# Kernel tuning notes

Hardware: AMD Instinct MI355X
Metric: run time of the kernel (lower is better)

## Reference

```python
import jax, jax.numpy as jnp
import numpy as np

N_NODES, N_EDGES, F_IN = 8192, 32768, 16
N_SUB, N_GRAPH = 512, 32
EDGE_DIM, HID = 5, 128
DIMS = [(16, 32), (32, 64), (64, 64)]  # (M_in, M_out) per NNConv layer


def _segment_mean(x, seg, n):
    s = jax.ops.segment_sum(x, seg, num_segments=n)
    c = jax.ops.segment_sum(jnp.ones((x.shape[0], 1), x.dtype), seg, num_segments=n)
    return s / jnp.maximum(c, 1.0)


def _nnconv(x, src, dst, eattr, W1, b1, W2, b2, root, bias):
    # edge MLP -> per-edge weight matrix theta: [E, M_in, M_out]
    h = jax.nn.relu(eattr @ W1 + b1)
    theta = (h @ W2 + b2).reshape(-1, x.shape[1], root.shape[1])
    msg = jnp.einsum('ei,eio->eo', x[src], theta)          # gather + per-edge matvec
    agg = jax.ops.segment_sum(msg, dst, num_segments=x.shape[0])  # scatter-add (aggr='add')
    return agg + x @ root + bias


def setup_inputs() -> dict:
    key = jax.random.key(0)
    ks = jax.random.split(key, 32)
    inp = {}
    inp['x'] = jax.random.normal(ks[0], (N_NODES, F_IN), jnp.float32)
    inp['edge_index'] = jax.random.randint(ks[1], (2, N_EDGES), 0, N_NODES)
    inp['edge_attr'] = jax.random.uniform(ks[2], (N_EDGES, EDGE_DIM), jnp.float32)
    inp['node_to_subgraph'] = jnp.sort(jax.random.randint(ks[3], (N_NODES,), 0, N_SUB))
    inp['subgraph_to_graph'] = jnp.sort(jax.random.randint(ks[4], (N_SUB,), 0, N_GRAPH))
    i = 5
    for l, (ci, co) in enumerate(DIMS):
        inp[f'W1_{l}'] = jax.random.normal(ks[i], (EDGE_DIM, HID), jnp.float32) * 0.1
        inp[f'b1_{l}'] = jnp.zeros((HID,), jnp.float32)
        inp[f'W2_{l}'] = jax.random.normal(ks[i + 1], (HID, ci * co), jnp.float32) * 0.05
        inp[f'b2_{l}'] = jnp.zeros((ci * co,), jnp.float32)
        inp[f'root_{l}'] = jax.random.normal(ks[i + 2], (ci, co), jnp.float32) * 0.1
        inp[f'bias_{l}'] = jnp.zeros((co,), jnp.float32)
        i += 3
    inp['fc1_w'] = jax.random.normal(ks[i], (64, 32), jnp.float32) * 0.1
    inp['fc1_b'] = jnp.zeros((32,), jnp.float32)
    inp['fc2_w'] = jax.random.normal(ks[i + 1], (32, 16), jnp.float32) * 0.1
    inp['fc2_b'] = jnp.zeros((16,), jnp.float32)
    inp['fc3_w'] = jax.random.normal(ks[i + 2], (16, 1), jnp.float32) * 0.1
    inp['fc3_b'] = jnp.zeros((1,), jnp.float32)
    return inp


def reference(x, edge_index, edge_attr, node_to_subgraph, subgraph_to_graph,
              W1_0, b1_0, W2_0, b2_0, root_0, bias_0,
              W1_1, b1_1, W2_1, b2_1, root_1, bias_1,
              W1_2, b1_2, W2_2, b2_2, root_2, bias_2,
              fc1_w, fc1_b, fc2_w, fc2_b, fc3_w, fc3_b):
    src, dst = edge_index[0], edge_index[1]
    layers = [(W1_0, b1_0, W2_0, b2_0, root_0, bias_0),
              (W1_1, b1_1, W2_1, b2_1, root_1, bias_1),
              (W1_2, b1_2, W2_2, b2_2, root_2, bias_2)]
    h = x
    for (W1, b1, W2, b2, root, bias) in layers:
        h = jax.nn.elu(_nnconv(h, src, dst, edge_attr, W1, b1, W2, b2, root, bias))
    h = _segment_mean(h, node_to_subgraph, N_SUB)      # global_mean_pool over subgraphs
    h = _segment_mean(h, subgraph_to_graph, N_GRAPH)   # global_mean_pool over graphs
    h = jax.nn.elu(h @ fc1_w + fc1_b)
    h = jax.nn.elu(h @ fc2_w + fc2_b)
    return (h @ fc3_w + fc3_b).reshape(-1)
```

## Files before the change

kernel.cpp:

```cpp
#include <hip/hip_runtime.h>

#define E_EDGES 32768
#define NN 8192
#define HID 128
#define KS 4

typedef _Float16 half8 __attribute__((ext_vector_type(8)));
typedef _Float16 half4 __attribute__((ext_vector_type(4)));
typedef float f32x4 __attribute__((ext_vector_type(4)));

__global__ void csr_scan_k(const int* __restrict__ dst, float* __restrict__ pools,
                           int npool, int* __restrict__ roff, int* __restrict__ cursor) {
  __shared__ int h[NN];
  __shared__ int ps[1024];
  int t = threadIdx.x;
  for (int j = t; j < NN; j += 1024) h[j] = 0;
  for (int j = t; j < npool; j += 1024) pools[j] = 0.f;
  __syncthreads();
  for (int j = t; j < E_EDGES; j += 1024) atomicAdd(&h[dst[j]], 1);
  __syncthreads();
  int loc[8]; int s = 0;
  int base = t * 8;
#pragma unroll
  for (int j = 0; j < 8; ++j) { loc[j] = s; s += h[base + j]; }
  ps[t] = s;
  __syncthreads();
  for (int off = 1; off < 1024; off <<= 1) {
    int v = 0;
    if (t >= off) v = ps[t - off];
    __syncthreads();
    if (t >= off) ps[t] += v;
    __syncthreads();
  }
  int excl = (t == 0) ? 0 : ps[t - 1];
#pragma unroll
  for (int j = 0; j < 8; ++j) { int v = excl + loc[j]; roff[base + j] = v; cursor[base + j] = v; }
  if (t == 1023) roff[NN] = ps[1023];
}

__global__ void scatter_k(const int* __restrict__ dst, int* __restrict__ cursor, int* __restrict__ eidx) {
  int e = blockIdx.x * 256 + threadIdx.x;
  if (e < E_EDGES) { int p = atomicAdd(&cursor[dst[e]], 1); eidx[p] = e; }
}

__device__ __forceinline__ void prep_one(int idx, int l2ci, int l2co,
                                         const float* __restrict__ W2,
                                         const float* __restrict__ b2,
                                         _Float16* __restrict__ out) {
  int CI = 1 << l2ci, CO = 1 << l2co;
  int Kmain = CI << 7;
  int j = idx & 7;
  int n = (idx >> 3) & (CO - 1);
  int kg = idx >> (3 + l2co);
  int k = kg * 8 + j;
  float v = 0.f;
  if (k < Kmain) {
    int hh = k >> l2ci, i = k & (CI - 1);
    v = W2[((hh << l2ci) + i) * CO + n];
  } else if (k < Kmain + CI) {
    v = b2[(k - Kmain) * CO + n];
  }
  out[idx] = (_Float16)v;
}

__global__ void prep_all_k(const float* __restrict__ W2a, const float* __restrict__ b2a, _Float16* __restrict__ oa,
                           const float* __restrict__ W2b, const float* __restrict__ b2b, _Float16* __restrict__ ob,
                           const float* __restrict__ W2c, const float* __restrict__ b2c, _Float16* __restrict__ oc) {
  const int s0 = 2176 * 32, s1 = 4224 * 64, s2 = 8320 * 64;
  int idx = blockIdx.x * 256 + threadIdx.x;
  if (idx < s0) prep_one(idx, 4, 5, W2a, b2a, oa);
  else if (idx < s0 + s1) prep_one(idx - s0, 5, 6, W2b, b2b, ob);
  else if (idx < s0 + s1 + s2) prep_one(idx - s0 - s1, 6, 6, W2c, b2c, oc);
}

template <int CI, int CO>
__launch_bounds__(256, 2)
__global__ void msg_mfma_k(const float* __restrict__ xcur, const int* __restrict__ src,
                           const float* __restrict__ eattr, const float* __restrict__ W1,
                           const float* __restrict__ b1, const _Float16* __restrict__ Bsw,
                           float* __restrict__ msgbuf) {
  constexpr int ME = 256;
  constexpr int L2CI = (CI == 64) ? 6 : ((CI == 32) ? 5 : 4);
  constexpr int Kmain = 128 * CI;
  constexpr int SPLITK = 32 * CI;
  constexpr int TAILK = ((SPLITK + CI + 127) / 128) * 128;
  constexpr int XSTR = CI + 8;
  constexpr int FC = CO / 16;
  constexpr int C4 = CI / 4;
  constexpr int L2C4 = L2CI - 2;
  constexpr int NV = (CI == 64) ? 2 : 1;

  __shared__ _Float16 he_s[32 * ME];
  __shared__ _Float16 xs_s[ME * XSTR];
  __shared__ float ea_s[ME * 5];
  __shared__ float W1s[5 * 32];
  __shared__ float b1s[32];
  __shared__ int src_s[ME];

  int t = threadIdx.x;
  int e0 = blockIdx.x * ME;
  int y = blockIdx.y;
  int hbeg = y * 32;

  for (int j = t; j < ME * 5; j += 256) ea_s[j] = eattr[e0 * 5 + j];
  if (t < 5 * 32) W1s[t] = W1[(t >> 5) * HID + hbeg + (t & 31)];
  if (t < 32) b1s[t] = b1[hbeg + t];
  src_s[t] = src[e0 + t];
  __syncthreads();

  for (int j = t; j < 32 * ME; j += 256) {
    int hl = j / ME, e = j & (ME - 1);
    float v = b1s[hl];
#pragma unroll
    for (int d = 0; d < 5; ++d) v += ea_s[e * 5 + d] * W1s[d * 32 + hl];
    he_s[hl * ME + e] = (_Float16)fmaxf(v, 0.f);
  }
  for (int j = t; j < ME * C4; j += 256) {
    int e = j >> L2C4, i4 = j & (C4 - 1);
    float4 v = ((const float4*)xcur)[src_s[e] * C4 + i4];
    half4 hq = {(_Float16)v.x, (_Float16)v.y, (_Float16)v.z, (_Float16)v.w};
    *(half4*)&xs_s[e * XSTR + i4 * 4] = hq;
  }
  __syncthreads();

  int lane = t & 63;
  int w = t >> 6;
  int quad = lane >> 4, l15 = lane & 15;

  half8 xreg[4][NV];
#pragma unroll
  for (int fr = 0; fr < 4; ++fr)
#pragma unroll
    for (int v = 0; v < NV; ++v)
      xreg[fr][v] = *(const half8*)&xs_s[(w * 64 + fr * 16 + l15) * XSTR +
                                         ((quad * 8 + v * 32) & (CI - 1))];

  int cbeg = y * (SPLITK / 32);
  int cend = cbeg + ((y < 3) ? (SPLITK / 32) : (TAILK / 32));
  int nrounds = (cend - cbeg) >> 2;

  const half8* bsw8 = (const half8*)Bsw;
  int ib = quad * CO + l15;

  f32x4 acc[4][FC];
#pragma unroll
  for (int fr = 0; fr < 4; ++fr)
#pragma unroll
    for (int fc = 0; fc < FC; ++fc)
#pragma unroll
      for (int r = 0; r < 4; ++r) acc[fr][fc][r] = 0.f;

  half8 breg[4][FC];
#pragma unroll
  for (int j = 0; j < 4; ++j)
#pragma unroll
    for (int fc = 0; fc < FC; ++fc)
      breg[j][fc] = bsw8[(cbeg + j) * 4 * CO + ib + fc * 16];

  for (int r = 0; r < nrounds; ++r) {
#pragma unroll
    for (int j = 0; j < 4; ++j) {
      int c = cbeg + r * 4 + j;
      int kq = c * 32 + quad * 8;
      int hr = (kq >> L2CI) - hbeg;
      constexpr int PAR = (CI == 64) ? 1 : 0;
      int vi = PAR ? (j & 1) : 0;
      half8 a[4];
#pragma unroll
      for (int fr = 0; fr < 4; ++fr) {
        int e = w * 64 + fr * 16 + l15;
        _Float16 hv = (_Float16)1.f;
        if (kq < Kmain) hv = he_s[hr * ME + e];
        a[fr] = xreg[fr][vi] * hv;
      }
#pragma unroll
      for (int fc = 0; fc < FC; ++fc) {
#pragma unroll
        for (int fr = 0; fr < 4; ++fr)
          acc[fr][fc] = __builtin_amdgcn_mfma_f32_16x16x32_f16(a[fr], breg[j][fc], acc[fr][fc], 0, 0, 0);
      }
      int cn = c + 4;
      if (cn >= cend) cn = cend - 1;
#pragma unroll
      for (int fc = 0; fc < FC; ++fc)
        breg[j][fc] = bsw8[cn * 4 * CO + ib + fc * 16];
    }
  }

  float* mb = msgbuf + ((size_t)y * E_EDGES + e0) * CO;
#pragma unroll
  for (int fr = 0; fr < 4; ++fr)
#pragma unroll
    for (int fc = 0; fc < FC; ++fc)
#pragma unroll
      for (int r = 0; r < 4; ++r) {
        int el = w * 64 + fr * 16 + quad * 4 + r;
        int o = fc * 16 + l15;
        mb[el * CO + o] = acc[fr][fc][r];
      }
}

template <int CI, int CO>
__global__ void gather_elu_k(const float* __restrict__ xcur, const float* __restrict__ root,
                             const float* __restrict__ bias, const float* __restrict__ msgbuf,
                             const int* __restrict__ roff, const int* __restrict__ eidx,
                             float* __restrict__ xnext) {
  constexpr int NB = 256 / CO;
  __shared__ float xs[NB * CI];
  int t = threadIdx.x;
  int n0 = blockIdx.x * NB;
  for (int j = t; j < NB * CI; j += 256) xs[j] = xcur[n0 * CI + j];
  __syncthreads();
  int nl = t / CO, o = t & (CO - 1);
  int n = n0 + nl;
  float a = bias[o];
#pragma unroll
  for (int i = 0; i < CI; ++i) a += xs[nl * CI + i] * root[i * CO + o];
  int j1 = roff[n + 1];
  for (int j = roff[n]; j < j1; ++j) {
    int e = eidx[j];
    float m = 0.f;
#pragma unroll
    for (int s = 0; s < KS; ++s) m += msgbuf[((size_t)s * E_EDGES + e) * CO + o];
    a += m;
  }
  xnext[n * CO + o] = a > 0.f ? a : expm1f(a);
}

__global__ void pool_sub_k(const float* __restrict__ x3, const int* __restrict__ n2s,
                           float* __restrict__ ssum, float* __restrict__ scnt) {
  int idx = blockIdx.x * 256 + threadIdx.x;
  int n = idx >> 6, o = idx & 63;
  int s = n2s[n];
  atomicAdd(&ssum[(s << 6) + o], x3[idx]);
  if (o == 0) atomicAdd(&scnt[s], 1.f);
}

__global__ void pool_graph_k(const float* __restrict__ ssum, const float* __restrict__ scnt,
                             const int* __restrict__ s2g, float* __restrict__ gsum,
                             float* __restrict__ gcnt) {
  int idx = blockIdx.x * 256 + threadIdx.x;
  int s = idx >> 6, o = idx & 63;
  int g = s2g[s];
  float v = ssum[idx] / fmaxf(scnt[s], 1.f);
  atomicAdd(&gsum[(g << 6) + o], v);
  if (o == 0) atomicAdd(&gcnt[g], 1.f);
}

__global__ void head_k(const float* __restrict__ gsum, const float* __restrict__ gcnt,
                       const float* __restrict__ w1, const float* __restrict__ b1,
                       const float* __restrict__ w2, const float* __restrict__ b2,
                       const float* __restrict__ w3, const float* __restrict__ b3,
                       float* __restrict__ out) {
  int g = blockIdx.x;
  int t = threadIdx.x;
  __shared__ float m[64], s1[32], s2[16];
  float c = fmaxf(gcnt[g], 1.f);
  m[t] = gsum[g * 64 + t] / c;
  __syncthreads();
  if (t < 32) {
    float a = b1[t];
    for (int i = 0; i < 64; ++i) a += m[i] * w1[i * 32 + t];
    s1[t] = a > 0.f ? a : expm1f(a);
  }
  __syncthreads();
  if (t < 16) {
    float a = b2[t];
    for (int i = 0; i < 32; ++i) a += s1[i] * w2[i * 16 + t];
    s2[t] = a > 0.f ? a : expm1f(a);
  }
  __syncthreads();
  if (t == 0) {
    float a = b3[0];
    for (int i = 0; i < 16; ++i) a += s2[i] * w3[i];
    out[g] = a;
  }
}

extern "C" void kernel_launch(void* const* d_in, const int* in_sizes, int n_in,
                              void* d_out, int out_size, void* d_ws, size_t ws_size,
                              hipStream_t stream) {
  (void)in_sizes; (void)n_in; (void)out_size; (void)ws_size;
  const float* x0 = (const float*)d_in[0];
  const int* ei = (const int*)d_in[1];
  const float* ea = (const float*)d_in[2];
  const int* n2s = (const int*)d_in[3];
  const int* s2g = (const int*)d_in[4];
  const float* W1_[3] = {(const float*)d_in[5], (const float*)d_in[11], (const float*)d_in[17]};
  const float* b1_[3] = {(const float*)d_in[6], (const float*)d_in[12], (const float*)d_in[18]};
  const float* W2_[3] = {(const float*)d_in[7], (const float*)d_in[13], (const float*)d_in[19]};
  const float* b2_[3] = {(const float*)d_in[8], (const float*)d_in[14], (const float*)d_in[20]};
  const float* rt_[3] = {(const float*)d_in[9], (const float*)d_in[15], (const float*)d_in[21]};
  const float* bs_[3] = {(const float*)d_in[10], (const float*)d_in[16], (const float*)d_in[22]};
  const float* fc1w = (const float*)d_in[23]; const float* fc1b = (const float*)d_in[24];
  const float* fc2w = (const float*)d_in[25]; const float* fc2b = (const float*)d_in[26];
  const float* fc3w = (const float*)d_in[27]; const float* fc3b = (const float*)d_in[28];
  float* out = (float*)d_out;

  const int* srcp = ei;
  const int* dstp = ei + E_EDGES;

  char* wsb = (char*)d_ws;
  size_t off = 0;
  auto alloc = [&](size_t bytes) {
    void* p = wsb + off;
    off += (bytes + 255) & ~(size_t)255;
    return p;
  };
  _Float16* Bsw0 = (_Float16*)alloc((size_t)2176 * 32 * 2);
  _Float16* Bsw1 = (_Float16*)alloc((size_t)4224 * 64 * 2);
  _Float16* Bsw2 = (_Float16*)alloc((size_t)8320 * 64 * 2);
  float* msgbuf = (float*)alloc((size_t)KS * E_EDGES * 64 * 4);
  float* x1 = (float*)alloc((size_t)NN * 32 * 4);
  float* x2 = (float*)alloc((size_t)NN * 64 * 4);
  float* x3 = (float*)alloc((size_t)NN * 64 * 4);
  int* roff = (int*)alloc((size_t)(NN + 1) * 4);
  int* cursor = (int*)alloc((size_t)NN * 4);
  int* eidx = (int*)alloc((size_t)E_EDGES * 4);
  const int npool = 512 * 64 + 512 + 32 * 64 + 32;
  float* pools = (float*)alloc((size_t)npool * 4);
  float* ssum = pools;
  float* scnt = pools + 512 * 64;
  float* gsum = scnt + 512;
  float* gcnt = gsum + 32 * 64;

  csr_scan_k<<<1, 1024, 0, stream>>>(dstp, pools, npool, roff, cursor);
  scatter_k<<<E_EDGES / 256, 256, 0, stream>>>(dstp, cursor, eidx);
  const int preptot = 2176 * 32 + 4224 * 64 + 8320 * 64;
  prep_all_k<<<(preptot + 255) / 256, 256, 0, stream>>>(W2_[0], b2_[0], Bsw0,
                                                        W2_[1], b2_[1], Bsw1,
                                                        W2_[2], b2_[2], Bsw2);

  dim3 mg(E_EDGES / 256, KS);
  msg_mfma_k<16, 32><<<mg, 256, 0, stream>>>(x0, srcp, ea, W1_[0], b1_[0], Bsw0, msgbuf);
  gather_elu_k<16, 32><<<NN / 8, 256, 0, stream>>>(x0, rt_[0], bs_[0], msgbuf, roff, eidx, x1);
  msg_mfma_k<32, 64><<<mg, 256, 0, stream>>>(x1, srcp, ea, W1_[1], b1_[1], Bsw1, msgbuf);
  gather_elu_k<32, 64><<<NN / 4, 256, 0, stream>>>(x1, rt_[1], bs_[1], msgbuf, roff, eidx, x2);
  msg_mfma_k<64, 64><<<mg, 256, 0, stream>>>(x2, srcp, ea, W1_[2], b1_[2], Bsw2, msgbuf);
  gather_elu_k<64, 64><<<NN / 4, 256, 0, stream>>>(x2, rt_[2], bs_[2], msgbuf, roff, eidx, x3);

  pool_sub_k<<<NN * 64 / 256, 256, 0, stream>>>(x3, n2s, ssum, scnt);
  pool_graph_k<<<512 * 64 / 256, 256, 0, stream>>>(ssum, scnt, s2g, gsum, gcnt);
  head_k<<<32, 64, 0, stream>>>(gsum, gcnt, fc1w, fc1b, fc2w, fc2b, fc3w, fc3b, out);
}
```

Before: 271.1 us.

## Replace CSR gather with atomic scatter-add from MFMA message kernel, fuse pooling and head

Drops the CSR build (histogram scan plus scatter) and the split-K message buffer. The MFMA message kernel now atomically adds its per-edge results straight into per-layer node aggregation buffers indexed by dst. The finalize kernel reads the aggregate, adds the root term and applies ELU. On the last layer it atomically pools into subgraph sums, and one final kernel computes counts by binary search and runs the graph pooling and MLP head. The aim is to cut kernel launches and msgbuf write/read traffic, at the cost of many global float atomics (4 split-K partial writes per output element) and non-deterministic summation order.

```diff
diff --git a/kernel.cpp b/kernel.cpp
--- a/kernel.cpp
+++ b/kernel.cpp
@@ -3,45 +3,10 @@
 #define E_EDGES 32768
 #define NN 8192
 #define HID 128
-#define KS 4
 
 typedef _Float16 half8 __attribute__((ext_vector_type(8)));
 typedef _Float16 half4 __attribute__((ext_vector_type(4)));
 typedef float f32x4 __attribute__((ext_vector_type(4)));
-
-__global__ void csr_scan_k(const int* __restrict__ dst, float* __restrict__ pools,
-                           int npool, int* __restrict__ roff, int* __restrict__ cursor) {
-  __shared__ int h[NN];
-  __shared__ int ps[1024];
-  int t = threadIdx.x;
-  for (int j = t; j < NN; j += 1024) h[j] = 0;
-  for (int j = t; j < npool; j += 1024) pools[j] = 0.f;
-  __syncthreads();
-  for (int j = t; j < E_EDGES; j += 1024) atomicAdd(&h[dst[j]], 1);
-  __syncthreads();
-  int loc[8]; int s = 0;
-  int base = t * 8;
-#pragma unroll
-  for (int j = 0; j < 8; ++j) { loc[j] = s; s += h[base + j]; }
-  ps[t] = s;
-  __syncthreads();
-  for (int off = 1; off < 1024; off <<= 1) {
-    int v = 0;
-    if (t >= off) v = ps[t - off];
-    __syncthreads();
-    if (t >= off) ps[t] += v;
-    __syncthreads();
-  }
-  int excl = (t == 0) ? 0 : ps[t - 1];
-#pragma unroll
-  for (int j = 0; j < 8; ++j) { int v = excl + loc[j]; roff[base + j] = v; cursor[base + j] = v; }
-  if (t == 1023) roff[NN] = ps[1023];
-}
-
-__global__ void scatter_k(const int* __restrict__ dst, int* __restrict__ cursor, int* __restrict__ eidx) {
-  int e = blockIdx.x * 256 + threadIdx.x;
-  if (e < E_EDGES) { int p = atomicAdd(&cursor[dst[e]], 1); eidx[p] = e; }
-}
 
 __device__ __forceinline__ void prep_one(int idx, int l2ci, int l2co,
                                          const float* __restrict__ W2,
@@ -63,22 +28,29 @@
   out[idx] = (_Float16)v;
 }
 
-__global__ void prep_all_k(const float* __restrict__ W2a, const float* __restrict__ b2a, _Float16* __restrict__ oa,
-                           const float* __restrict__ W2b, const float* __restrict__ b2b, _Float16* __restrict__ ob,
-                           const float* __restrict__ W2c, const float* __restrict__ b2c, _Float16* __restrict__ oc) {
-  const int s0 = 2176 * 32, s1 = 4224 * 64, s2 = 8320 * 64;
+#define ZTOT (8192 * 32 + 8192 * 64 + 8192 * 64 + 512 * 64)
+#define PREP0 (2176 * 32)
+#define PREP1 (4224 * 64)
+#define PREP2 (8320 * 64)
+
+__global__ void prep_k(float* __restrict__ zr,
+                       const float* __restrict__ W2a, const float* __restrict__ b2a, _Float16* __restrict__ oa,
+                       const float* __restrict__ W2b, const float* __restrict__ b2b, _Float16* __restrict__ ob,
+                       const float* __restrict__ W2c, const float* __restrict__ b2c, _Float16* __restrict__ oc) {
   int idx = blockIdx.x * 256 + threadIdx.x;
-  if (idx < s0) prep_one(idx, 4, 5, W2a, b2a, oa);
-  else if (idx < s0 + s1) prep_one(idx - s0, 5, 6, W2b, b2b, ob);
-  else if (idx < s0 + s1 + s2) prep_one(idx - s0 - s1, 6, 6, W2c, b2c, oc);
+  if (idx < ZTOT) { zr[idx] = 0.f; return; }
+  idx -= ZTOT;
+  if (idx < PREP0) prep_one(idx, 4, 5, W2a, b2a, oa);
+  else if (idx < PREP0 + PREP1) prep_one(idx - PREP0, 5, 6, W2b, b2b, ob);
+  else if (idx < PREP0 + PREP1 + PREP2) prep_one(idx - PREP0 - PREP1, 6, 6, W2c, b2c, oc);
 }
 
 template <int CI, int CO>
 __launch_bounds__(256, 2)
 __global__ void msg_mfma_k(const float* __restrict__ xcur, const int* __restrict__ src,
-                           const float* __restrict__ eattr, const float* __restrict__ W1,
-                           const float* __restrict__ b1, const _Float16* __restrict__ Bsw,
-                           float* __restrict__ msgbuf) {
+                           const int* __restrict__ dst, const float* __restrict__ eattr,
+                           const float* __restrict__ W1, const float* __restrict__ b1,
+                           const _Float16* __restrict__ Bsw, float* __restrict__ agg) {
   constexpr int ME = 256;
   constexpr int L2CI = (CI == 64) ? 6 : ((CI == 32) ? 5 : 4);
   constexpr int Kmain = 128 * CI;
@@ -96,6 +68,7 @@
   __shared__ float W1s[5 * 32];
   __shared__ float b1s[32];
   __shared__ int src_s[ME];
+  __shared__ int dst_s[ME];
 
   int t = threadIdx.x;
   int e0 = blockIdx.x * ME;
@@ -106,10 +79,11 @@
   if (t < 5 * 32) W1s[t] = W1[(t >> 5) * HID + hbeg + (t & 31)];
   if (t < 32) b1s[t] = b1[hbeg + t];
   src_s[t] = src[e0 + t];
+  dst_s[t] = dst[e0 + t];
   __syncthreads();
 
   for (int j = t; j < 32 * ME; j += 256) {
-    int hl = j / ME, e = j & (ME - 1);
+    int hl = j >> 8, e = j & (ME - 1);
     float v = b1s[hl];
 #pragma unroll
     for (int d = 0; d < 5; ++d) v += ea_s[e * 5 + d] * W1s[d * 32 + hl];
@@ -162,15 +136,14 @@
     for (int j = 0; j < 4; ++j) {
       int c = cbeg + r * 4 + j;
       int kq = c * 32 + quad * 8;
-      int hr = (kq >> L2CI) - hbeg;
+      int hr = (kq < Kmain) ? ((kq >> L2CI) - hbeg) : 0;
       constexpr int PAR = (CI == 64) ? 1 : 0;
       int vi = PAR ? (j & 1) : 0;
       half8 a[4];
 #pragma unroll
       for (int fr = 0; fr < 4; ++fr) {
         int e = w * 64 + fr * 16 + l15;
-        _Float16 hv = (_Float16)1.f;
-        if (kq < Kmain) hv = he_s[hr * ME + e];
+        _Float16 hv = (kq < Kmain) ? he_s[hr * ME + e] : (_Float16)1.f;
         a[fr] = xreg[fr][vi] * hv;
       }
 #pragma unroll
@@ -187,24 +160,24 @@
     }
   }
 
-  float* mb = msgbuf + ((size_t)y * E_EDGES + e0) * CO;
 #pragma unroll
   for (int fr = 0; fr < 4; ++fr)
 #pragma unroll
-    for (int fc = 0; fc < FC; ++fc)
-#pragma unroll
-      for (int r = 0; r < 4; ++r) {
-        int el = w * 64 + fr * 16 + quad * 4 + r;
-        int o = fc * 16 + l15;
-        mb[el * CO + o] = acc[fr][fc][r];
-      }
-}
-
-template <int CI, int CO>
-__global__ void gather_elu_k(const float* __restrict__ xcur, const float* __restrict__ root,
-                             const float* __restrict__ bias, const float* __restrict__ msgbuf,
-                             const int* __restrict__ roff, const int* __restrict__ eidx,
-                             float* __restrict__ xnext) {
+    for (int r = 0; r < 4; ++r) {
+      int el = w * 64 + fr * 16 + quad * 4 + r;
+      int d = dst_s[el];
+      float* base = agg + (size_t)d * CO + l15;
+#pragma unroll
+      for (int fc = 0; fc < FC; ++fc)
+        atomicAdd(base + fc * 16, acc[fr][fc][r]);
+    }
+}
+
+template <int CI, int CO, bool POOL>
+__global__ void fin_k(const float* __restrict__ xcur, const float* __restrict__ root,
+                      const float* __restrict__ bias, const float* __restrict__ agg,
+                      const int* __restrict__ n2s, float* __restrict__ ssum,
+                      float* __restrict__ xnext) {
   constexpr int NB = 256 / CO;
   __shared__ float xs[NB * CI];
   int t = threadIdx.x;
@@ -213,67 +186,62 @@
   __syncthreads();
   int nl = t / CO, o = t & (CO - 1);
   int n = n0 + nl;
-  float a = bias[o];
+  float a = bias[o] + agg[n * CO + o];
 #pragma unroll
   for (int i = 0; i < CI; ++i) a += xs[nl * CI + i] * root[i * CO + o];
-  int j1 = roff[n + 1];
-  for (int j = roff[n]; j < j1; ++j) {
-    int e = eidx[j];
-    float m = 0.f;
-#pragma unroll
-    for (int s = 0; s < KS; ++s) m += msgbuf[((size_t)s * E_EDGES + e) * CO + o];
-    a += m;
-  }
-  xnext[n * CO + o] = a > 0.f ? a : expm1f(a);
-}
-
-__global__ void pool_sub_k(const float* __restrict__ x3, const int* __restrict__ n2s,
-                           float* __restrict__ ssum, float* __restrict__ scnt) {
-  int idx = blockIdx.x * 256 + threadIdx.x;
-  int n = idx >> 6, o = idx & 63;
-  int s = n2s[n];
-  atomicAdd(&ssum[(s << 6) + o], x3[idx]);
-  if (o == 0) atomicAdd(&scnt[s], 1.f);
-}
-
-__global__ void pool_graph_k(const float* __restrict__ ssum, const float* __restrict__ scnt,
-                             const int* __restrict__ s2g, float* __restrict__ gsum,
-                             float* __restrict__ gcnt) {
-  int idx = blockIdx.x * 256 + threadIdx.x;
-  int s = idx >> 6, o = idx & 63;
-  int g = s2g[s];
-  float v = ssum[idx] / fmaxf(scnt[s], 1.f);
-  atomicAdd(&gsum[(g << 6) + o], v);
-  if (o == 0) atomicAdd(&gcnt[g], 1.f);
-}
-
-__global__ void head_k(const float* __restrict__ gsum, const float* __restrict__ gcnt,
-                       const float* __restrict__ w1, const float* __restrict__ b1,
-                       const float* __restrict__ w2, const float* __restrict__ b2,
-                       const float* __restrict__ w3, const float* __restrict__ b3,
-                       float* __restrict__ out) {
-  int g = blockIdx.x;
+  float r = a > 0.f ? a : expm1f(a);
+  if (POOL) atomicAdd(&ssum[(n2s[n] << 6) + o], r);
+  else xnext[n * CO + o] = r;
+}
+
+__device__ __forceinline__ int lbound(const int* __restrict__ a, int n, int v) {
+  int lo = 0, hi = n;
+  while (lo < hi) { int m = (lo + hi) >> 1; if (a[m] < v) lo = m + 1; else hi = m; }
+  return lo;
+}
+
+__global__ void final_k(const float* __restrict__ ssum, const int* __restrict__ n2s,
+                        const int* __restrict__ s2g,
+                        const float* __restrict__ w1, const float* __restrict__ b1,
+                        const float* __restrict__ w2, const float* __restrict__ b2,
+                        const float* __restrict__ w3, const float* __restrict__ b3,
+                        float* __restrict__ out) {
+  __shared__ float gsum[32 * 64];
+  __shared__ float cnt_s[512];
+  __shared__ float gcnt[32];
+  __shared__ float s1[32 * 32];
+  __shared__ float s2[32 * 16];
   int t = threadIdx.x;
-  __shared__ float m[64], s1[32], s2[16];
-  float c = fmaxf(gcnt[g], 1.f);
-  m[t] = gsum[g * 64 + t] / c;
+  for (int j = t; j < 32 * 64; j += 1024) gsum[j] = 0.f;
+  if (t < 512) cnt_s[t] = (float)(lbound(n2s, NN, t + 1) - lbound(n2s, NN, t));
+  if (t < 32) gcnt[t] = (float)(lbound(s2g, 512, t + 1) - lbound(s2g, 512, t));
+  __syncthreads();
+  for (int j = t; j < 512 * 64; j += 1024) {
+    int s = j >> 6, o = j & 63;
+    float v = ssum[j] / fmaxf(cnt_s[s], 1.f);
+    atomicAdd(&gsum[(s2g[s] << 6) + o], v);
+  }
+  __syncthreads();
+  for (int j = t; j < 2048; j += 1024) gsum[j] /= fmaxf(gcnt[j >> 6], 1.f);
+  __syncthreads();
+  {
+    int g = t >> 5, jj = t & 31;
+    float a = b1[jj];
+    for (int i = 0; i < 64; ++i) a += gsum[(g << 6) + i] * w1[i * 32 + jj];
+    s1[(g << 5) + jj] = a > 0.f ? a : expm1f(a);
+  }
+  __syncthreads();
+  if (t < 512) {
+    int g = t >> 4, jj = t & 15;
+    float a = b2[jj];
+    for (int i = 0; i < 32; ++i) a += s1[(g << 5) + i] * w2[i * 16 + jj];
+    s2[(g << 4) + jj] = a > 0.f ? a : expm1f(a);
+  }
   __syncthreads();
   if (t < 32) {
-    float a = b1[t];
-    for (int i = 0; i < 64; ++i) a += m[i] * w1[i * 32 + t];
-    s1[t] = a > 0.f ? a : expm1f(a);
-  }
-  __syncthreads();
-  if (t < 16) {
-    float a = b2[t];
-    for (int i = 0; i < 32; ++i) a += s1[i] * w2[i * 16 + t];
-    s2[t] = a > 0.f ? a : expm1f(a);
-  }
-  __syncthreads();
-  if (t == 0) {
     float a = b3[0];
-    for (int i = 0; i < 16; ++i) a += s2[i] * w3[i];
-    out[g] = a;
+    for (int i = 0; i < 16; ++i) a += s2[(t << 4) + i] * w3[i];
+    out[t] = a;
   }
 }
 
@@ -307,39 +275,28 @@
     off += (bytes + 255) & ~(size_t)255;
     return p;
   };
-  _Float16* Bsw0 = (_Float16*)alloc((size_t)2176 * 32 * 2);
-  _Float16* Bsw1 = (_Float16*)alloc((size_t)4224 * 64 * 2);
-  _Float16* Bsw2 = (_Float16*)alloc((size_t)8320 * 64 * 2);
-  float* msgbuf = (float*)alloc((size_t)KS * E_EDGES * 64 * 4);
+  _Float16* Bsw0 = (_Float16*)alloc((size_t)PREP0 * 2);
+  _Float16* Bsw1 = (_Float16*)alloc((size_t)PREP1 * 2);
+  _Float16* Bsw2 = (_Float16*)alloc((size_t)PREP2 * 2);
+  float* agg1 = (float*)alloc((size_t)NN * 32 * 4);
+  float* agg2 = (float*)alloc((size_t)NN * 64 * 4);
+  float* agg3 = (float*)alloc((size_t)NN * 64 * 4);
+  float* ssum = (float*)alloc((size_t)512 * 64 * 4);
   float* x1 = (float*)alloc((size_t)NN * 32 * 4);
   float* x2 = (float*)alloc((size_t)NN * 64 * 4);
-  float* x3 = (float*)alloc((size_t)NN * 64 * 4);
-  int* roff = (int*)alloc((size_t)(NN + 1) * 4);
-  int* cursor = (int*)alloc((size_t)NN * 4);
-  int* eidx = (int*)alloc((size_t)E_EDGES * 4);
-  const int npool = 512 * 64 + 512 + 32 * 64 + 32;
-  float* pools = (float*)alloc((size_t)npool * 4);
-  float* ssum = pools;
-  float* scnt = pools + 512 * 64;
-  float* gsum = scnt + 512;
-  float* gcnt = gsum + 32 * 64;
-
-  csr_scan_k<<<1, 1024, 0, stream>>>(dstp, pools, npool, roff, cursor);
-  scatter_k<<<E_EDGES / 256, 256, 0, stream>>>(dstp, cursor, eidx);
-  const int preptot = 2176 * 32 + 4224 * 64 + 8320 * 64;
-  prep_all_k<<<(preptot + 255) / 256, 256, 0, stream>>>(W2_[0], b2_[0], Bsw0,
-                                                        W2_[1], b2_[1], Bsw1,
-                                                        W2_[2], b2_[2], Bsw2);
-
-  dim3 mg(E_EDGES / 256, KS);
-  msg_mfma_k<16, 32><<<mg, 256, 0, stream>>>(x0, srcp, ea, W1_[0], b1_[0], Bsw0, msgbuf);
-  gather_elu_k<16, 32><<<NN / 8, 256, 0, stream>>>(x0, rt_[0], bs_[0], msgbuf, roff, eidx, x1);
-  msg_mfma_k<32, 64><<<mg, 256, 0, stream>>>(x1, srcp, ea, W1_[1], b1_[1], Bsw1, msgbuf);
-  gather_elu_k<32, 64><<<NN / 4, 256, 0, stream>>>(x1, rt_[1], bs_[1], msgbuf, roff, eidx, x2);
-  msg_mfma_k<64, 64><<<mg, 256, 0, stream>>>(x2, srcp, ea, W1_[2], b1_[2], Bsw2, msgbuf);
-  gather_elu_k<64, 64><<<NN / 4, 256, 0, stream>>>(x2, rt_[2], bs_[2], msgbuf, roff, eidx, x3);
-
-  pool_sub_k<<<NN * 64 / 256, 256, 0, stream>>>(x3, n2s, ssum, scnt);
-  pool_graph_k<<<512 * 64 / 256, 256, 0, stream>>>(ssum, scnt, s2g, gsum, gcnt);
-  head_k<<<32, 64, 0, stream>>>(gsum, gcnt, fc1w, fc1b, fc2w, fc2b, fc3w, fc3b, out);
-}
+
+  const int preptot = ZTOT + PREP0 + PREP1 + PREP2;
+  prep_k<<<(preptot + 255) / 256, 256, 0, stream>>>(agg1, W2_[0], b2_[0], Bsw0,
+                                                    W2_[1], b2_[1], Bsw1,
+                                                    W2_[2], b2_[2], Bsw2);
+
+  dim3 mg(E_EDGES / 256, 4);
+  msg_mfma_k<16, 32><<<mg, 256, 0, stream>>>(x0, srcp, dstp, ea, W1_[0], b1_[0], Bsw0, agg1);
+  fin_k<16, 32, false><<<NN / 8, 256, 0, stream>>>(x0, rt_[0], bs_[0], agg1, n2s, ssum, x1);
+  msg_mfma_k<32, 64><<<mg, 256, 0, stream>>>(x1, srcp, dstp, ea, W1_[1], b1_[1], Bsw1, agg2);
+  fin_k<32, 64, false><<<NN / 4, 256, 0, stream>>>(x1, rt_[1], bs_[1], agg2, n2s, ssum, x2);
+  msg_mfma_k<64, 64><<<mg, 256, 0, stream>>>(x2, srcp, dstp, ea, W1_[2], b1_[2], Bsw2, agg3);
+  fin_k<64, 64, true><<<NN / 4, 256, 0, stream>>>(x2, rt_[2], bs_[2], agg3, n2s, ssum, nullptr);
+
+  final_k<<<1, 1024, 0, stream>>>(ssum, n2s, s2g, fc1w, fc1b, fc2w, fc2b, fc3w, fc3b, out);
+}
```

Measured after the change: 308.0 us. 1.14x slower.
